# Kernel optimization log

Measured on AMD Instinct MI355X. Metric: run time of the kernel, lower is better.

Reference implementation:

```python
import jax, jax.numpy as jnp
import numpy as np

HEADS = 16
SEQ_LEN = 2048
EMB = 1024
BATCH = 2


def setup_inputs() -> dict:
    key = jax.random.key(0)
    ks = jax.random.split(key, 5)
    s = 1.0 / np.sqrt(EMB)
    return {
        "x": jax.random.normal(ks[0], (BATCH, SEQ_LEN, EMB), dtype=jnp.float32),
        "Wk": jax.random.normal(ks[1], (EMB, EMB), dtype=jnp.float32) * s,
        "Wq": jax.random.normal(ks[2], (EMB, EMB), dtype=jnp.float32) * s,
        "Wv": jax.random.normal(ks[3], (EMB, EMB), dtype=jnp.float32) * s,
        "Wu": jax.random.normal(ks[4], (EMB, EMB), dtype=jnp.float32) * s,
        "bu": jnp.zeros((EMB,), dtype=jnp.float32),
    }


def reference(x, Wk, Wq, Wv, Wu, bu):
    B, S, E = x.shape
    H = HEADS
    D = E // H
    # projections (torch Linear: y = x @ W.T); split heads -> [B, H, S, D]
    def proj(W):
        return (x @ W.T).reshape(B, S, H, D).transpose(0, 2, 1, 3)
    q, k, v = proj(Wq), proj(Wk), proj(Wv)
    scores = jnp.einsum("bhsd,bhtd->bhst", q, k) / jnp.sqrt(jnp.float32(D))
    causal_mask = jnp.triu(jnp.ones((S, S), dtype=bool), k=1)  # True above diag
    scores = jnp.where(causal_mask, -jnp.inf, scores)
    attn = jax.nn.softmax(scores, axis=-1)
    ctx = jnp.einsum("bhst,bhtd->bhsd", attn, v)  # [B,H,S,D]
    out = ctx.transpose(0, 2, 1, 3).reshape(B, S, E)
    return out @ Wu.T + bu
```

## Files before the change

kernel.cpp:

```cpp
#include <hip/hip_runtime.h>
#include <hip/hip_bf16.h>

#define HEADS 16
#define SEQ   2048
#define EMB   1024
#define BATCH 2
#define DHEAD 64
#define MTOK  (BATCH * SEQ)

typedef __bf16 bf16x8 __attribute__((ext_vector_type(8)));
typedef float  floatx4 __attribute__((ext_vector_type(4)));

__device__ __forceinline__ void gl_lds16(const void* g, void* l) {
  __builtin_amdgcn_global_load_lds((__attribute__((address_space(1))) void*)(g),
                                   (__attribute__((address_space(3))) void*)(l), 16, 0, 0);
}

__device__ __forceinline__ unsigned short f2bf(float f) {
  __bf16 h = (__bf16)f;
  return __builtin_bit_cast(unsigned short, h);
}

__global__ __launch_bounds__(256) void cvt_kernel(
    const float* __restrict__ x,  const float* __restrict__ wq,
    const float* __restrict__ wk, const float* __restrict__ wv,
    const float* __restrict__ wu,
    unsigned short* __restrict__ xb,  unsigned short* __restrict__ wqb,
    unsigned short* __restrict__ wkb, unsigned short* __restrict__ wvb,
    unsigned short* __restrict__ wub) {
  const int g = blockIdx.x * 256 + threadIdx.x;
  const int XG = (MTOK * EMB) / 4;
  const int WG = (EMB * EMB) / 4;
  const float* src; unsigned short* dst; int off;
  if (g < XG) { src = x; dst = xb; off = g; }
  else {
    int t = g - XG; int wsel = t / WG; off = t - wsel * WG;
    const float* ss[4] = {wq, wk, wv, wu};
    unsigned short* dd[4] = {wqb, wkb, wvb, wub};
    src = ss[wsel]; dst = dd[wsel];
  }
  float4 v = ((const float4*)src)[off];
  ushort4 o;
  o.x = f2bf(v.x); o.y = f2bf(v.y); o.z = f2bf(v.z); o.w = f2bf(v.w);
  ((ushort4*)dst)[off] = o;
}

__global__ __launch_bounds__(256) void gemm_qkv(
    const unsigned short* __restrict__ xb,
    const unsigned short* __restrict__ wqb, const unsigned short* __restrict__ wkb,
    const unsigned short* __restrict__ wvb,
    unsigned short* __restrict__ Qb, unsigned short* __restrict__ Kb,
    unsigned short* __restrict__ Vt) {
  constexpr int BM = 128, BN = 64, BK = 64;
  __shared__ unsigned short As[BM * BK];
  __shared__ unsigned short Bs[3 * BN * BK];
  const int m0 = blockIdx.x * BM, n0 = blockIdx.y * BN;
  const int tid = threadIdx.x, w = tid >> 6, lane = tid & 63;
  const int quad = lane >> 4, l16 = lane & 15;
  const int wm = w >> 1, wn = w & 1;
  const int srow = lane >> 3;
  const int scol = ((lane & 7) ^ srow) * 8;
  const unsigned short* Ws[3] = {wqb, wkb, wvb};

  floatx4 acc[3][4][2] = {};

  for (int kt = 0; kt < EMB / BK; ++kt) {
    const int k0 = kt * BK;
#pragma unroll
    for (int i = 0; i < 4; ++i) {
      int r0 = i * 32 + w * 8;
      gl_lds16(xb + (size_t)(m0 + r0 + srow) * EMB + k0 + scol, &As[r0 * BK]);
    }
#pragma unroll
    for (int z = 0; z < 3; ++z)
#pragma unroll
      for (int i = 0; i < 2; ++i) {
        int r0 = i * 32 + w * 8;
        gl_lds16(Ws[z] + (size_t)(n0 + r0 + srow) * EMB + k0 + scol,
                 &Bs[z * (BN * BK) + r0 * BK]);
      }
    __syncthreads();
#pragma unroll
    for (int ks = 0; ks < 2; ++ks) {
      bf16x8 af[4];
#pragma unroll
      for (int mb = 0; mb < 4; ++mb) {
        int ra = wm * 64 + mb * 16 + l16;
        af[mb] = *(const bf16x8*)&As[ra * BK + (((ks * 4 + quad) ^ (ra & 7)) * 8)];
      }
#pragma unroll
      for (int z = 0; z < 3; ++z) {
        bf16x8 bfv[2];
#pragma unroll
        for (int nb = 0; nb < 2; ++nb) {
          int rb = wn * 32 + nb * 16 + l16;
          bfv[nb] = *(const bf16x8*)&Bs[z * (BN * BK) + rb * BK + (((ks * 4 + quad) ^ (rb & 7)) * 8)];
        }
#pragma unroll
        for (int mb = 0; mb < 4; ++mb)
#pragma unroll
          for (int nb = 0; nb < 2; ++nb)
            acc[z][mb][nb] = __builtin_amdgcn_mfma_f32_16x16x32_bf16(af[mb], bfv[nb], acc[z][mb][nb], 0, 0, 0);
      }
    }
    __syncthreads();
  }

#pragma unroll
  for (int z = 0; z < 2; ++z) {
    unsigned short* C = (z == 0) ? Qb : Kb;
    const float scale = (z == 0) ? 0.180336876f : 1.0f;
#pragma unroll
    for (int mb = 0; mb < 4; ++mb) {
#pragma unroll
      for (int nb = 0; nb < 2; ++nb) {
        int n = n0 + wn * 32 + nb * 16 + l16;
#pragma unroll
        for (int r = 0; r < 4; ++r) {
          int m = m0 + wm * 64 + mb * 16 + quad * 4 + r;
          C[(size_t)m * EMB + n] = f2bf(acc[z][mb][nb][r] * scale);
        }
      }
    }
  }
#pragma unroll
  for (int mb = 0; mb < 4; ++mb) {
    int mbase = m0 + wm * 64 + mb * 16 + quad * 4;
    int b = mbase >> 11, s = mbase & (SEQ - 1);
#pragma unroll
    for (int nb = 0; nb < 2; ++nb) {
      int n = n0 + wn * 32 + nb * 16 + l16;
      ushort4 o;
      o.x = f2bf(acc[2][mb][nb][0]); o.y = f2bf(acc[2][mb][nb][1]);
      o.z = f2bf(acc[2][mb][nb][2]); o.w = f2bf(acc[2][mb][nb][3]);
      *(ushort4*)&Vt[((size_t)b * (HEADS * DHEAD) + n) * SEQ + s] = o;
    }
  }
}

__global__ __launch_bounds__(256) void attn_kernel(
    const unsigned short* __restrict__ Qb, const unsigned short* __restrict__ Kb,
    const unsigned short* __restrict__ Vt, unsigned short* __restrict__ ctx) {
  constexpr int KT = 64;
  constexpr int PST = KT + 12;
  __shared__ unsigned short Ks[KT * DHEAD];
  __shared__ unsigned short Vs[DHEAD * KT];
  __shared__ __bf16 Ps[4 * 16 * PST];
  const int qt = 31 - blockIdx.x, bh = blockIdx.y;
  const int b = bh >> 4, h = bh & 15;
  const int q0 = qt * 64;
  const int tid = threadIdx.x, w = tid >> 6, lane = tid & 63;
  const int quad = lane >> 4, l16 = lane & 15;

  const unsigned short* Kbh = Kb + (size_t)b * SEQ * EMB + h * DHEAD;
  const unsigned short* Vbh = Vt + (size_t)bh * DHEAD * SEQ;
  __bf16* Pw = &Ps[w * (16 * PST)];

  const int krow = w * 16 + l16;
  const int dc0 = quad * 8, dc1 = 32 + quad * 8;

  const int myrow = q0 + w * 16 + quad * 4;
  const size_t qrow = (size_t)(b * SEQ + q0 + w * 16 + l16) * EMB + h * DHEAD;
  bf16x8 qf[2];
  qf[0] = *(const bf16x8*)&Qb[qrow + quad * 8];
  qf[1] = *(const bf16x8*)&Qb[qrow + 32 + quad * 8];

  float lsum[4] = {0.0f, 0.0f, 0.0f, 0.0f};
  floatx4 acc_o[4] = {};

  const int nkt = qt + 1;
  for (int ktile = 0; ktile < nkt; ++ktile) {
    const int kt0 = ktile * KT;
    gl_lds16(Kbh + (size_t)(kt0 + krow) * EMB + dc0, &Ks[(w * 64 + lane) * 8]);
    gl_lds16(Kbh + (size_t)(kt0 + krow) * EMB + dc1, &Ks[((4 + w) * 64 + lane) * 8]);
    gl_lds16(Vbh + (size_t)krow * SEQ + kt0 + dc0, &Vs[(w * 64 + lane) * 8]);
    gl_lds16(Vbh + (size_t)krow * SEQ + kt0 + dc1, &Vs[((4 + w) * 64 + lane) * 8]);
    __syncthreads();

    floatx4 accs[4] = {};
#pragma unroll
    for (int ks = 0; ks < 2; ++ks)
#pragma unroll
      for (int nb = 0; nb < 4; ++nb) {
        bf16x8 kf = *(const bf16x8*)&Ks[((ks * 4 + nb) * 64 + lane) * 8];
        accs[nb] = __builtin_amdgcn_mfma_f32_16x16x32_bf16(qf[ks], kf, accs[nb], 0, 0, 0);
      }

    if (ktile == nkt - 1) {
#pragma unroll
      for (int nb = 0; nb < 4; ++nb) {
        int col = kt0 + nb * 16 + l16;
#pragma unroll
        for (int r = 0; r < 4; ++r)
          if (col > myrow + r) accs[nb][r] = -1e30f;
      }
    }

#pragma unroll
    for (int r = 0; r < 4; ++r) {
#pragma unroll
      for (int nb = 0; nb < 4; ++nb) {
        float pe = exp2f(accs[nb][r]);
        Pw[(quad * 4 + r) * PST + nb * 16 + l16] = (__bf16)pe;
        lsum[r] += pe;
      }
    }

#pragma unroll
    for (int ks = 0; ks < 2; ++ks) {
      bf16x8 pf = *(const bf16x8*)&Pw[l16 * PST + ks * 32 + quad * 8];
#pragma unroll
      for (int nb = 0; nb < 4; ++nb) {
        bf16x8 vf = *(const bf16x8*)&Vs[((ks * 4 + nb) * 64 + lane) * 8];
        acc_o[nb] = __builtin_amdgcn_mfma_f32_16x16x32_bf16(pf, vf, acc_o[nb], 0, 0, 0);
      }
    }
    __syncthreads();
  }

#pragma unroll
  for (int r = 0; r < 4; ++r) {
    float rs = lsum[r];
    rs += __shfl_xor(rs, 1);
    rs += __shfl_xor(rs, 2);
    rs += __shfl_xor(rs, 4);
    rs += __shfl_xor(rs, 8);
    float inv = 1.0f / rs;
    size_t base = (size_t)(b * SEQ + myrow + r) * EMB + h * DHEAD;
#pragma unroll
    for (int nb = 0; nb < 4; ++nb)
      ctx[base + nb * 16 + l16] = f2bf(acc_o[nb][r] * inv);
  }
}

__global__ __launch_bounds__(256) void gemm_out(
    const unsigned short* __restrict__ ctx, const unsigned short* __restrict__ wub,
    const float* __restrict__ bu, float* __restrict__ out) {
  constexpr int BM = 128, BN = 64, BK = 64;
  __shared__ unsigned short As[BM * BK];
  __shared__ unsigned short Bs[BN * BK];
  const int m0 = blockIdx.x * BM, n0 = blockIdx.y * BN;
  const int tid = threadIdx.x, w = tid >> 6, lane = tid & 63;
  const int quad = lane >> 4, l16 = lane & 15;
  const int wm = w >> 1, wn = w & 1;
  const int srow = lane >> 3;
  const int scol = ((lane & 7) ^ srow) * 8;

  floatx4 acc[4][2] = {};

  for (int kt = 0; kt < EMB / BK; ++kt) {
    const int k0 = kt * BK;
#pragma unroll
    for (int i = 0; i < 4; ++i) {
      int r0 = i * 32 + w * 8;
      gl_lds16(ctx + (size_t)(m0 + r0 + srow) * EMB + k0 + scol, &As[r0 * BK]);
    }
#pragma unroll
    for (int i = 0; i < 2; ++i) {
      int r0 = i * 32 + w * 8;
      gl_lds16(wub + (size_t)(n0 + r0 + srow) * EMB + k0 + scol, &Bs[r0 * BK]);
    }
    __syncthreads();
    bf16x8 af[4][2], bfv[2][2];
#pragma unroll
    for (int mb = 0; mb < 4; ++mb) {
      int ra = wm * 64 + mb * 16 + l16;
#pragma unroll
      for (int ks = 0; ks < 2; ++ks)
        af[mb][ks] = *(const bf16x8*)&As[ra * BK + (((ks * 4 + quad) ^ (ra & 7)) * 8)];
    }
#pragma unroll
    for (int nb = 0; nb < 2; ++nb) {
      int rb = wn * 32 + nb * 16 + l16;
#pragma unroll
      for (int ks = 0; ks < 2; ++ks)
        bfv[nb][ks] = *(const bf16x8*)&Bs[rb * BK + (((ks * 4 + quad) ^ (rb & 7)) * 8)];
    }
#pragma unroll
    for (int ks = 0; ks < 2; ++ks)
#pragma unroll
      for (int mb = 0; mb < 4; ++mb)
#pragma unroll
        for (int nb = 0; nb < 2; ++nb)
          acc[mb][nb] = __builtin_amdgcn_mfma_f32_16x16x32_bf16(af[mb][ks], bfv[nb][ks], acc[mb][nb], 0, 0, 0);
    __syncthreads();
  }

#pragma unroll
  for (int mb = 0; mb < 4; ++mb) {
#pragma unroll
    for (int nb = 0; nb < 2; ++nb) {
      int n = n0 + wn * 32 + nb * 16 + l16;
      float bias = bu[n];
#pragma unroll
      for (int r = 0; r < 4; ++r) {
        int m = m0 + wm * 64 + mb * 16 + quad * 4 + r;
        out[(size_t)m * EMB + n] = acc[mb][nb][r] + bias;
      }
    }
  }
}

extern "C" void kernel_launch(void* const* d_in, const int* in_sizes, int n_in,
                              void* d_out, int out_size, void* d_ws, size_t ws_size,
                              hipStream_t stream) {
  const float* x  = (const float*)d_in[0];
  const float* Wk = (const float*)d_in[1];
  const float* Wq = (const float*)d_in[2];
  const float* Wv = (const float*)d_in[3];
  const float* Wu = (const float*)d_in[4];
  const float* bu = (const float*)d_in[5];

  char* ws = (char*)d_ws;
  const size_t MB1 = 1 << 20;
  unsigned short* xb  = (unsigned short*)(ws + 0);
  unsigned short* wqb = (unsigned short*)(ws + 8  * MB1);
  unsigned short* wkb = (unsigned short*)(ws + 10 * MB1);
  unsigned short* wvb = (unsigned short*)(ws + 12 * MB1);
  unsigned short* wub = (unsigned short*)(ws + 14 * MB1);
  unsigned short* Qb  = (unsigned short*)(ws + 16 * MB1);
  unsigned short* Kb  = (unsigned short*)(ws + 24 * MB1);
  unsigned short* Vt  = (unsigned short*)(ws + 32 * MB1);
  unsigned short* ctx = (unsigned short*)(ws + 40 * MB1);

  cvt_kernel<<<8192, 256, 0, stream>>>(x, Wq, Wk, Wv, Wu, xb, wqb, wkb, wvb, wub);
  gemm_qkv<<<dim3(32, 16), 256, 0, stream>>>(xb, wqb, wkb, wvb, Qb, Kb, Vt);
  attn_kernel<<<dim3(32, 32), 256, 0, stream>>>(Qb, Kb, Vt, ctx);
  gemm_out<<<dim3(32, 16), 256, 0, stream>>>(ctx, wub, bu, (float*)d_out);
}
```

Baseline: 219.8 us.

## Load K/V fragments directly to registers per wave and drop block barriers

```diff
diff --git a/kernel.cpp b/kernel.cpp
--- a/kernel.cpp
+++ b/kernel.cpp
@@ -141,52 +141,55 @@
 __global__ __launch_bounds__(256) void attn_kernel(
     const unsigned short* __restrict__ Qb, const unsigned short* __restrict__ Kb,
     const unsigned short* __restrict__ Vt, unsigned short* __restrict__ ctx) {
-  constexpr int KT = 64;
-  constexpr int PST = KT + 12;
-  __shared__ unsigned short Ks[KT * DHEAD];
-  __shared__ unsigned short Vs[DHEAD * KT];
+  constexpr int PST = 76;
   __shared__ __bf16 Ps[4 * 16 * PST];
-  const int qt = 31 - blockIdx.x, bh = blockIdx.y;
+  const int g = blockIdx.x;
+  const int bh = g & 31;
   const int b = bh >> 4, h = bh & 15;
-  const int q0 = qt * 64;
   const int tid = threadIdx.x, w = tid >> 6, lane = tid & 63;
   const int quad = lane >> 4, l16 = lane & 15;
+  const int rg = 127 - ((g >> 5) * 4 + w);
+  const int nkt = (rg >> 2) + 1;
 
   const unsigned short* Kbh = Kb + (size_t)b * SEQ * EMB + h * DHEAD;
   const unsigned short* Vbh = Vt + (size_t)bh * DHEAD * SEQ;
   __bf16* Pw = &Ps[w * (16 * PST)];
 
-  const int krow = w * 16 + l16;
-  const int dc0 = quad * 8, dc1 = 32 + quad * 8;
-
-  const int myrow = q0 + w * 16 + quad * 4;
-  const size_t qrow = (size_t)(b * SEQ + q0 + w * 16 + l16) * EMB + h * DHEAD;
+  const int myrow = rg * 16 + quad * 4;
+  const size_t qoff = (size_t)(b * SEQ + rg * 16 + l16) * EMB + h * DHEAD;
   bf16x8 qf[2];
-  qf[0] = *(const bf16x8*)&Qb[qrow + quad * 8];
-  qf[1] = *(const bf16x8*)&Qb[qrow + 32 + quad * 8];
+  qf[0] = *(const bf16x8*)&Qb[qoff + quad * 8];
+  qf[1] = *(const bf16x8*)&Qb[qoff + 32 + quad * 8];
 
   float lsum[4] = {0.0f, 0.0f, 0.0f, 0.0f};
   floatx4 acc_o[4] = {};
 
-  const int nkt = qt + 1;
-  for (int ktile = 0; ktile < nkt; ++ktile) {
-    const int kt0 = ktile * KT;
-    gl_lds16(Kbh + (size_t)(kt0 + krow) * EMB + dc0, &Ks[(w * 64 + lane) * 8]);
-    gl_lds16(Kbh + (size_t)(kt0 + krow) * EMB + dc1, &Ks[((4 + w) * 64 + lane) * 8]);
-    gl_lds16(Vbh + (size_t)krow * SEQ + kt0 + dc0, &Vs[(w * 64 + lane) * 8]);
-    gl_lds16(Vbh + (size_t)krow * SEQ + kt0 + dc1, &Vs[((4 + w) * 64 + lane) * 8]);
-    __syncthreads();
+  for (int kt = 0; kt < nkt; ++kt) {
+    const int kt0 = kt * 64;
+    const unsigned short* Kt = Kbh + (size_t)(kt0 + l16) * EMB + quad * 8;
+    bf16x8 kf[8];
+#pragma unroll
+    for (int ks = 0; ks < 2; ++ks)
+#pragma unroll
+      for (int nb = 0; nb < 4; ++nb)
+        kf[ks * 4 + nb] = *(const bf16x8*)(Kt + (size_t)nb * (16 * EMB) + ks * 32);
 
     floatx4 accs[4] = {};
 #pragma unroll
     for (int ks = 0; ks < 2; ++ks)
 #pragma unroll
-      for (int nb = 0; nb < 4; ++nb) {
-        bf16x8 kf = *(const bf16x8*)&Ks[((ks * 4 + nb) * 64 + lane) * 8];
-        accs[nb] = __builtin_amdgcn_mfma_f32_16x16x32_bf16(qf[ks], kf, accs[nb], 0, 0, 0);
-      }
-
-    if (ktile == nkt - 1) {
+      for (int nb = 0; nb < 4; ++nb)
+        accs[nb] = __builtin_amdgcn_mfma_f32_16x16x32_bf16(qf[ks], kf[ks * 4 + nb], accs[nb], 0, 0, 0);
+
+    const unsigned short* Vt0 = Vbh + (size_t)l16 * SEQ + kt0 + quad * 8;
+    bf16x8 vf[8];
+#pragma unroll
+    for (int ks = 0; ks < 2; ++ks)
+#pragma unroll
+      for (int nb = 0; nb < 4; ++nb)
+        vf[ks * 4 + nb] = *(const bf16x8*)(Vt0 + (size_t)nb * (16 * SEQ) + ks * 32);
+
+    if (kt == nkt - 1) {
 #pragma unroll
       for (int nb = 0; nb < 4; ++nb) {
         int col = kt0 + nb * 16 + l16;
@@ -197,25 +200,21 @@
     }
 
 #pragma unroll
-    for (int r = 0; r < 4; ++r) {
+    for (int r = 0; r < 4; ++r)
 #pragma unroll
       for (int nb = 0; nb < 4; ++nb) {
         float pe = exp2f(accs[nb][r]);
         Pw[(quad * 4 + r) * PST + nb * 16 + l16] = (__bf16)pe;
         lsum[r] += pe;
       }
-    }
 
 #pragma unroll
     for (int ks = 0; ks < 2; ++ks) {
       bf16x8 pf = *(const bf16x8*)&Pw[l16 * PST + ks * 32 + quad * 8];
 #pragma unroll
-      for (int nb = 0; nb < 4; ++nb) {
-        bf16x8 vf = *(const bf16x8*)&Vs[((ks * 4 + nb) * 64 + lane) * 8];
-        acc_o[nb] = __builtin_amdgcn_mfma_f32_16x16x32_bf16(pf, vf, acc_o[nb], 0, 0, 0);
-      }
-    }
-    __syncthreads();
+      for (int nb = 0; nb < 4; ++nb)
+        acc_o[nb] = __builtin_amdgcn_mfma_f32_16x16x32_bf16(pf, vf[ks * 4 + nb], acc_o[nb], 0, 0, 0);
+    }
   }
 
 #pragma unroll
@@ -325,6 +324,6 @@
 
   cvt_kernel<<<8192, 256, 0, stream>>>(x, Wq, Wk, Wv, Wu, xb, wqb, wkb, wvb, wub);
   gemm_qkv<<<dim3(32, 16), 256, 0, stream>>>(xb, wqb, wkb, wvb, Qb, Kb, Vt);
-  attn_kernel<<<dim3(32, 32), 256, 0, stream>>>(Qb, Kb, Vt, ctx);
+  attn_kernel<<<1024, 256, 0, stream>>>(Qb, Kb, Vt, ctx);
   gemm_out<<<dim3(32, 16), 256, 0, stream>>>(ctx, wub, bu, (float*)d_out);
 }
```

Result: slower. 274.1 us (+24.7%).
